# Optimization experiments

Measured on AMD Instinct MI355X. Metric: run time of the kernel, lower is better.

The kernel has to match this reference:

```python
import jax, jax.numpy as jnp
import numpy as np
import math

WINDOW_SIZE = 1024
CAUSAL = True


def setup_inputs() -> dict:
    key = jax.random.key(0)
    kq, kk, kv = jax.random.split(key, 3)
    B, H, L, D = 2, 16, 4096, 128
    q = jax.random.normal(kq, (B, H, L, D), dtype=jnp.float32)
    k = jax.random.normal(kk, (B, H, L, D), dtype=jnp.float32)
    v = jax.random.normal(kv, (B, H, L, D), dtype=jnp.float32)
    return {"q": q, "k": k, "v": v}


def _sliding_window_attention(q, k, v):
    # Faithful port of SlidingWindowAttention._blockwise_attention (L > 2048 path).
    B, H, L, D = q.shape
    block = min(WINDOW_SIZE, 1024)
    scale = 1.0 / math.sqrt(D)
    half_w = WINDOW_SIZE // 2
    outs = []
    # Python loop over a small fixed number of blocks (L/block = 4), not data dims.
    for s in range(0, L, block):
        e = min(s + block, L)
        ks = max(0, s - half_w)
        ke = min(L, e + half_w)
        if CAUSAL:
            ke = min(ke, e)
        qb = q[:, :, s:e, :]          # [B,H,Q,D]
        kb = k[:, :, ks:ke, :]        # [B,H,K,D]
        vb = v[:, :, ks:ke, :]        # [B,H,K,D]
        scores = jnp.einsum('bhqd,bhkd->bhqk', qb, kb) * scale
        if CAUSAL:
            qi = jnp.arange(s, e)[:, None]   # [Q,1]
            ki = jnp.arange(ks, ke)[None, :]  # [1,K]
            causal_mask = qi >= ki            # [Q,K]
            scores = jnp.where(causal_mask[None, None], scores, -jnp.inf)
        attn = jax.nn.softmax(scores, axis=-1)
        outs.append(jnp.einsum('bhqk,bhkd->bhqd', attn, vb))
    return jnp.concatenate(outs, axis=2)


def reference(q, k, v):
    return _sliding_window_attention(q, k, v)
```

## Files before the change

kernel.cpp:

```cpp
#include <hip/hip_runtime.h>
#include <hip/hip_bf16.h>
#include <stdint.h>

typedef __bf16 bf16_t;
typedef __bf16 bf16x8 __attribute__((ext_vector_type(8)));
typedef __bf16 bf16x4 __attribute__((ext_vector_type(4)));
typedef float f32x4 __attribute__((ext_vector_type(4)));

#define L_SEQ 4096
#define D_DIM 128
#define NBH   32
#define KT    64

__global__ __launch_bounds__(256)
void cvt_k(const float* __restrict__ Kg, bf16_t* __restrict__ Kws) {
    const int n   = blockIdx.x * 256 + threadIdx.x;
    const int key = n >> 4;
    const int pc  = n & 15;
    const int lc  = pc ^ (key & 7);
    const float* s = Kg + (size_t)key * D_DIM + lc * 8;
    f32x4 a = *(const f32x4*)(s);
    f32x4 b = *(const f32x4*)(s + 4);
    bf16x8 h;
    #pragma unroll
    for (int j = 0; j < 4; ++j) { h[j] = (bf16_t)a[j]; h[4 + j] = (bf16_t)b[j]; }
    *(bf16x8*)(Kws + (size_t)key * D_DIM + pc * 8) = h;
}

__global__ __launch_bounds__(256)
void cvt_v(const float* __restrict__ Vg, bf16_t* __restrict__ Vws) {
    const int blk  = blockIdx.x;
    const int bh   = blk >> 6;
    const int kb   = blk & 63;
    const int t    = threadIdx.x;
    const int d    = t & 127;
    const int half = t >> 7;
    const float* src0 = Vg + (size_t)(bh * L_SEQ + kb * 64) * D_DIM + d;
    bf16_t* dstrow = Vws + ((size_t)(bh * 64 + kb) * D_DIM + d) * 64;
    #pragma unroll
    for (int r2 = 0; r2 < 4; ++r2) {
        const int lc = half + 2 * r2;
        bf16x8 h;
        #pragma unroll
        for (int j = 0; j < 8; ++j)
            h[j] = (bf16_t)src0[(size_t)(lc * 8 + j) * D_DIM];
        const int pc = lc ^ (d & 7);
        *(bf16x8*)(&dstrow[pc * 8]) = h;
    }
}

__device__ __forceinline__ void ld_lds16(const void* g, void* s) {
    __builtin_amdgcn_global_load_lds(
        (const __attribute__((address_space(1))) unsigned int*)g,
        (__attribute__((address_space(3))) unsigned int*)s, 16, 0, 0);
}

#define QT2 128

__global__ __launch_bounds__(256, 2)
void swa_fwd2(const float* __restrict__ Qg,
              const bf16_t* __restrict__ Kws,
              const bf16_t* __restrict__ Vws,
              float* __restrict__ Og) {
    __shared__ __align__(16) bf16_t KtS[2][KT * D_DIM];
    __shared__ __align__(16) bf16_t VtS[2][D_DIM * KT];
    __shared__ __align__(16) bf16_t Pst[4][16 * KT];

    const int t    = threadIdx.x;
    const int w    = t >> 6;
    const int ln   = t & 15;
    const int quad = (t & 63) >> 4;
    const int l7   = t & 7;

    const int id = blockIdx.x;
    const int bh = id & 31;
    const int g  = id >> 5;
    const int r_ = g & 7;
    const int k_ = g >> 3;
    const int qt = 8 * k_ + ((k_ & 1) ? (7 - r_) : r_);

    const size_t baseF = (size_t)bh * L_SEQ * D_DIM;
    const float*  Qp = Qg + baseF;
    float*        Op = Og + baseF;
    const bf16_t* Kb = Kws + baseF;
    const bf16_t* Vb = Vws + (size_t)bh * 64 * D_DIM * 64;

    const int qbase  = qt * QT2;
    const int blk    = qbase & ~1023;
    const int kstart = (blk - 512) > 0 ? (blk - 512) : 0;
    const int kend   = qbase + QT2;
    const int ntile  = (kend - kstart) / KT;

    const float SC  = 0.08838834764831845f * 1.4426950408889634f;
    const float FIX = 8.0f;
    const float NEG = -1.0e30f;

    bf16x8 qf[2][4];
    #pragma unroll
    for (int mt = 0; mt < 2; ++mt) {
        const float* qrow = Qp + (size_t)(qbase + w * 32 + mt * 16 + ln) * D_DIM + quad * 8;
        #pragma unroll
        for (int ks = 0; ks < 4; ++ks) {
            f32x4 a = *(const f32x4*)(qrow + ks * 32);
            f32x4 b = *(const f32x4*)(qrow + ks * 32 + 4);
            bf16x8 q8;
            #pragma unroll
            for (int j = 0; j < 4; ++j) { q8[j] = (bf16_t)(a[j] * SC); q8[4 + j] = (bf16_t)(b[j] * SC); }
            qf[mt][ks] = q8;
        }
    }

    f32x4 Oacc[2][8];
    #pragma unroll
    for (int mt = 0; mt < 2; ++mt)
        #pragma unroll
        for (int dt = 0; dt < 8; ++dt) Oacc[mt][dt] = f32x4{0.f, 0.f, 0.f, 0.f};
    float lsum[2] = {0.f, 0.f};

    auto stage = [&](int b, int k0) {
        const char* ksrc = (const char*)Kb + (size_t)k0 * 256;
        const char* vsrc = (const char*)Vb + (size_t)(k0 >> 6) * 16384;
        char* kd = (char*)(&KtS[b][0]);
        char* vd = (char*)(&VtS[b][0]);
        #pragma unroll
        for (int i = 0; i < 4; ++i) {
            const int off = (i * 256 + t) * 16;
            ld_lds16(ksrc + off, kd + off);
            ld_lds16(vsrc + off, vd + off);
        }
    };

    stage(0, kstart);
    __syncthreads();

    int buf = 0;
    for (int kt = 0; kt < ntile; ++kt) {
        const int k0 = kstart + kt * KT;
        if (kt + 1 < ntile) stage(buf ^ 1, k0 + KT);

        f32x4 S[2][4];
        #pragma unroll
        for (int mt = 0; mt < 2; ++mt)
            #pragma unroll
            for (int nt = 0; nt < 4; ++nt) S[mt][nt] = f32x4{0.f, 0.f, 0.f, 0.f};
        #pragma unroll
        for (int ks = 0; ks < 4; ++ks) {
            #pragma unroll
            for (int nt = 0; nt < 4; ++nt) {
                const bf16x8 bk = *(const bf16x8*)(
                    &KtS[buf][(nt * 16 + ln) * D_DIM + (((quad + ks * 4) ^ l7) * 8)]);
                S[0][nt] = __builtin_amdgcn_mfma_f32_16x16x32_bf16(bk, qf[0][ks], S[0][nt], 0, 0, 0);
                S[1][nt] = __builtin_amdgcn_mfma_f32_16x16x32_bf16(bk, qf[1][ks], S[1][nt], 0, 0, 0);
            }
        }

        bf16x8 pa[2][2];
        #pragma unroll
        for (int mt = 0; mt < 2; ++mt) {
            const int qwm = qbase + w * 32 + mt * 16;
            const int qg  = qwm + ln;
            const bool nm = (k0 + KT - 1) > qwm;
            #pragma unroll
            for (int nt = 0; nt < 4; ++nt) {
                bf16x4 hp;
                #pragma unroll
                for (int r = 0; r < 4; ++r) {
                    float s = S[mt][nt][r];
                    if (nm) {
                        const int kg = k0 + nt * 16 + quad * 4 + r;
                        if (kg > qg) s = NEG;
                    }
                    const float e = __builtin_amdgcn_exp2f(s - FIX);
                    lsum[mt] += e;
                    hp[r] = (bf16_t)e;
                }
                *(bf16x4*)(&Pst[w][ln * 64 + (((nt * 2 + (quad >> 1)) ^ l7) * 8) + (quad & 1) * 4]) = hp;
            }
            #pragma unroll
            for (int ks2 = 0; ks2 < 2; ++ks2)
                pa[mt][ks2] = *(const bf16x8*)(
                    &Pst[w][ln * 64 + (((quad + ks2 * 4) ^ l7) * 8)]);
        }

        #pragma unroll
        for (int dt = 0; dt < 8; ++dt) {
            #pragma unroll
            for (int ks2 = 0; ks2 < 2; ++ks2) {
                const bf16x8 bv = *(const bf16x8*)(
                    &VtS[buf][(dt * 16 + ln) * 64 + (((quad + ks2 * 4) ^ l7) * 8)]);
                Oacc[0][dt] = __builtin_amdgcn_mfma_f32_16x16x32_bf16(bv, pa[0][ks2], Oacc[0][dt], 0, 0, 0);
                Oacc[1][dt] = __builtin_amdgcn_mfma_f32_16x16x32_bf16(bv, pa[1][ks2], Oacc[1][dt], 0, 0, 0);
            }
        }

        __syncthreads();
        buf ^= 1;
    }

    #pragma unroll
    for (int mt = 0; mt < 2; ++mt) {
        float l = lsum[mt];
        l += __shfl_xor(l, 16, 64);
        l += __shfl_xor(l, 32, 64);
        const float inv = (l > 0.f) ? (1.f / l) : 0.f;
        const int qg = qbase + w * 32 + mt * 16 + ln;
        float* orow = Op + (size_t)qg * D_DIM + quad * 4;
        #pragma unroll
        for (int dt = 0; dt < 8; ++dt) {
            f32x4 o = Oacc[mt][dt];
            #pragma unroll
            for (int j = 0; j < 4; ++j) o[j] *= inv;
            *(f32x4*)(orow + dt * 16) = o;
        }
    }
}

#define QT 64
#define LDK 136
#define LDV 72
#define LDP 72

__global__ __launch_bounds__(256, 2)
void swa_fwd(const float* __restrict__ Qg,
             const float* __restrict__ Kg,
             const float* __restrict__ Vg,
             float* __restrict__ Og) {
    __shared__ __align__(16) bf16_t Kt[KT][LDK];
    __shared__ __align__(16) bf16_t Vt[D_DIM][LDV];
    __shared__ __align__(16) bf16_t Pstf[4][16][LDP];

    const int t    = threadIdx.x;
    const int w    = t >> 6;
    const int ln   = t & 15;
    const int quad = (t & 63) >> 4;

    const int id = blockIdx.x;
    const int bh = id & 31;
    const int g  = id >> 5;
    const int q0 = g & 7;
    const int kk = g >> 3;
    const int qt = 16 * (kk >> 1) + ((kk & 1) ? (15 - q0) : q0);

    const size_t base = (size_t)bh * L_SEQ * D_DIM;
    const float* Qp = Qg + base;
    const float* Kp = Kg + base;
    const float* Vp = Vg + base;
    float*       Op = Og + base;

    const int qbase  = qt * QT;
    const int blk    = qbase & ~1023;
    const int kstart = (blk - 512) > 0 ? (blk - 512) : 0;
    const int kend   = qbase + QT;
    const int ntile  = (kend - kstart) / KT;

    const int qw = qbase + w * 16;

    const float SC  = 0.08838834764831845f * 1.4426950408889634f;
    const float FIX = 8.0f;

    bf16x8 qf[4];
    {
        const float* qrow = Qp + (size_t)(qw + ln) * D_DIM + quad * 8;
        #pragma unroll
        for (int ks = 0; ks < 4; ++ks) {
            f32x4 a = *(const f32x4*)(qrow + ks * 32);
            f32x4 b = *(const f32x4*)(qrow + ks * 32 + 4);
            bf16x8 q8;
            #pragma unroll
            for (int j = 0; j < 4; ++j) {
                q8[j]     = (bf16_t)(a[j] * SC);
                q8[4 + j] = (bf16_t)(b[j] * SC);
            }
            qf[ks] = q8;
        }
    }

    f32x4 Oacc[8];
    #pragma unroll
    for (int dt = 0; dt < 8; ++dt) Oacc[dt] = f32x4{0.f, 0.f, 0.f, 0.f};
    float lsum[4] = {0.f, 0.f, 0.f, 0.f};
    const float NEG = -1.0e30f;

    const int kr   = t >> 5;
    const int kc   = t & 31;
    const int vd   = t & 127;
    const int vkcb = t >> 7;

    f32x4 kreg[8];
    float vreg[4][8];

    auto load_tile = [&](int k0) {
        #pragma unroll
        for (int i = 0; i < 8; ++i)
            kreg[i] = *(const f32x4*)(Kp + (size_t)(k0 + kr + 8 * i) * D_DIM + kc * 4);
        #pragma unroll
        for (int r2 = 0; r2 < 4; ++r2) {
            const int kcc = vkcb + 2 * r2;
            #pragma unroll
            for (int j = 0; j < 8; ++j)
                vreg[r2][j] = Vp[(size_t)(k0 + kcc * 8 + j) * D_DIM + vd];
        }
    };
    auto store_tile = [&]() {
        #pragma unroll
        for (int i = 0; i < 8; ++i) {
            bf16x4 h;
            #pragma unroll
            for (int j = 0; j < 4; ++j) h[j] = (bf16_t)kreg[i][j];
            *(bf16x4*)(&Kt[kr + 8 * i][kc * 4]) = h;
        }
        #pragma unroll
        for (int r2 = 0; r2 < 4; ++r2) {
            const int kcc = vkcb + 2 * r2;
            bf16x8 h8;
            #pragma unroll
            for (int j = 0; j < 8; ++j) h8[j] = (bf16_t)vreg[r2][j];
            *(bf16x8*)(&Vt[vd][kcc * 8]) = h8;
        }
    };

    load_tile(kstart);

    for (int kt = 0; kt < ntile; ++kt) {
        const int k0 = kstart + kt * KT;
        __syncthreads();
        store_tile();
        __syncthreads();
        if (kt + 1 < ntile) load_tile(k0 + KT);

        f32x4 S[4];
        #pragma unroll
        for (int nt = 0; nt < 4; ++nt) S[nt] = f32x4{0.f, 0.f, 0.f, 0.f};
        #pragma unroll
        for (int ks = 0; ks < 4; ++ks) {
            #pragma unroll
            for (int nt = 0; nt < 4; ++nt) {
                bf16x8 bk = *(const bf16x8*)(&Kt[nt * 16 + ln][quad * 8 + ks * 32]);
                S[nt] = __builtin_amdgcn_mfma_f32_16x16x32_bf16(qf[ks], bk, S[nt], 0, 0, 0);
            }
        }

        const bool lastTile = (kt == ntile - 1);
        float p[4][4];
        #pragma unroll
        for (int nt = 0; nt < 4; ++nt) {
            #pragma unroll
            for (int r = 0; r < 4; ++r) {
                float s = S[nt][r];
                if (lastTile) {
                    const int kg = k0 + nt * 16 + ln;
                    const int qg = qw + quad * 4 + r;
                    if (kg > qg) s = NEG;
                }
                const float e = __builtin_amdgcn_exp2f(s - FIX);
                p[nt][r] = e;
                lsum[r] += e;
            }
        }

        #pragma unroll
        for (int nt = 0; nt < 4; ++nt)
            #pragma unroll
            for (int r = 0; r < 4; ++r)
                Pstf[w][quad * 4 + r][nt * 16 + ln] = (bf16_t)p[nt][r];

        bf16x8 pa[2];
        #pragma unroll
        for (int ks2 = 0; ks2 < 2; ++ks2)
            pa[ks2] = *(const bf16x8*)(&Pstf[w][ln][quad * 8 + ks2 * 32]);

        #pragma unroll
        for (int dt = 0; dt < 8; ++dt) {
            #pragma unroll
            for (int ks2 = 0; ks2 < 2; ++ks2) {
                bf16x8 bv = *(const bf16x8*)(&Vt[dt * 16 + ln][quad * 8 + ks2 * 32]);
                Oacc[dt] = __builtin_amdgcn_mfma_f32_16x16x32_bf16(pa[ks2], bv, Oacc[dt], 0, 0, 0);
            }
        }
    }

    #pragma unroll
    for (int r = 0; r < 4; ++r) {
        float l = lsum[r];
        #pragma unroll
        for (int msk = 1; msk < 16; msk <<= 1)
            l += __shfl_xor(l, msk, 64);
        const float inv = (l > 0.f) ? (1.f / l) : 0.f;
        const int qg = qw + quad * 4 + r;
        float* orow = Op + (size_t)qg * D_DIM + ln;
        #pragma unroll
        for (int dt = 0; dt < 8; ++dt)
            orow[dt * 16] = Oacc[dt][r] * inv;
    }
}

extern "C" void kernel_launch(void* const* d_in, const int* in_sizes, int n_in,
                              void* d_out, int out_size, void* d_ws, size_t ws_size,
                              hipStream_t stream) {
    const float* q = (const float*)d_in[0];
    const float* k = (const float*)d_in[1];
    const float* v = (const float*)d_in[2];
    float* o = (float*)d_out;

    const size_t kbytes = (size_t)NBH * L_SEQ * D_DIM * sizeof(bf16_t);
    if (d_ws && ws_size >= 2 * kbytes) {
        bf16_t* kws = (bf16_t*)d_ws;
        bf16_t* vws = (bf16_t*)((char*)d_ws + kbytes);
        cvt_k<<<dim3(8192), dim3(256), 0, stream>>>(k, kws);
        cvt_v<<<dim3(2048), dim3(256), 0, stream>>>(v, vws);
        swa_fwd2<<<dim3(1024), dim3(256), 0, stream>>>(q, kws, vws, o);
    } else {
        swa_fwd<<<dim3(2048), dim3(256), 0, stream>>>(q, k, v, o);
    }
}
```

Baseline: 306.8 us.

## Shrink key tile to 32, raise occupancy, skip fully masked wave tiles

Halves the key tile from 64 to 32 keys. This shrinks the shared-memory footprint and register pressure so four blocks per CU can be requested instead of two, and the V pre-transpose layout and its swizzle are changed to match. Each wave now skips compute on key tiles lying entirely above its causal diagonal, and MFMA phases are wrapped in s_setprio to favour matrix issue. The cost is twice as many tile iterations and barriers per block, with smaller staging loads that hide less latency per sync.

```diff
diff --git a/kernel.cpp b/kernel.cpp
--- a/kernel.cpp
+++ b/kernel.cpp
@@ -10,7 +10,7 @@
 #define L_SEQ 4096
 #define D_DIM 128
 #define NBH   32
-#define KT    64
+#define KT    32
 
 __global__ __launch_bounds__(256)
 void cvt_k(const float* __restrict__ Kg, bf16_t* __restrict__ Kws) {
@@ -30,22 +30,22 @@
 __global__ __launch_bounds__(256)
 void cvt_v(const float* __restrict__ Vg, bf16_t* __restrict__ Vws) {
     const int blk  = blockIdx.x;
-    const int bh   = blk >> 6;
-    const int kb   = blk & 63;
+    const int bh   = blk >> 7;
+    const int kb   = blk & 127;
     const int t    = threadIdx.x;
     const int d    = t & 127;
     const int half = t >> 7;
-    const float* src0 = Vg + (size_t)(bh * L_SEQ + kb * 64) * D_DIM + d;
-    bf16_t* dstrow = Vws + ((size_t)(bh * 64 + kb) * D_DIM + d) * 64;
-    #pragma unroll
-    for (int r2 = 0; r2 < 4; ++r2) {
+    const float* src0 = Vg + (size_t)(bh * L_SEQ + kb * 32) * D_DIM + d;
+    bf16_t* dstrow = Vws + ((size_t)(bh * 128 + kb) * D_DIM + d) * 32;
+    const int sw = (d >> 1) & 3;
+    #pragma unroll
+    for (int r2 = 0; r2 < 2; ++r2) {
         const int lc = half + 2 * r2;
         bf16x8 h;
         #pragma unroll
         for (int j = 0; j < 8; ++j)
             h[j] = (bf16_t)src0[(size_t)(lc * 8 + j) * D_DIM];
-        const int pc = lc ^ (d & 7);
-        *(bf16x8*)(&dstrow[pc * 8]) = h;
+        *(bf16x8*)(&dstrow[(lc ^ sw) * 8]) = h;
     }
 }
 
@@ -57,8 +57,8 @@
 
 #define QT2 128
 
-__global__ __launch_bounds__(256, 2)
-void swa_fwd2(const float* __restrict__ Qg,
+__global__ __launch_bounds__(256, 4)
+void swa_fwd3(const float* __restrict__ Qg,
               const bf16_t* __restrict__ Kws,
               const bf16_t* __restrict__ Vws,
               float* __restrict__ Og) {
@@ -83,7 +83,7 @@
     const float*  Qp = Qg + baseF;
     float*        Op = Og + baseF;
     const bf16_t* Kb = Kws + baseF;
-    const bf16_t* Vb = Vws + (size_t)bh * 64 * D_DIM * 64;
+    const bf16_t* Vb = Vws + (size_t)bh * 128 * D_DIM * 32;
 
     const int qbase  = qt * QT2;
     const int blk    = qbase & ~1023;
@@ -91,6 +91,9 @@
     const int kend   = qbase + QT2;
     const int ntile  = (kend - kstart) / KT;
 
+    const int qw    = qbase + w * 32;
+    const int qwmax = qw + 31;
+
     const float SC  = 0.08838834764831845f * 1.4426950408889634f;
     const float FIX = 8.0f;
     const float NEG = -1.0e30f;
@@ -98,7 +101,7 @@
     bf16x8 qf[2][4];
     #pragma unroll
     for (int mt = 0; mt < 2; ++mt) {
-        const float* qrow = Qp + (size_t)(qbase + w * 32 + mt * 16 + ln) * D_DIM + quad * 8;
+        const float* qrow = Qp + (size_t)(qw + mt * 16 + ln) * D_DIM + quad * 8;
         #pragma unroll
         for (int ks = 0; ks < 4; ++ks) {
             f32x4 a = *(const f32x4*)(qrow + ks * 32);
@@ -119,11 +122,11 @@
 
     auto stage = [&](int b, int k0) {
         const char* ksrc = (const char*)Kb + (size_t)k0 * 256;
-        const char* vsrc = (const char*)Vb + (size_t)(k0 >> 6) * 16384;
+        const char* vsrc = (const char*)Vb + (size_t)(k0 >> 5) * 8192;
         char* kd = (char*)(&KtS[b][0]);
         char* vd = (char*)(&VtS[b][0]);
         #pragma unroll
-        for (int i = 0; i < 4; ++i) {
+        for (int i = 0; i < 2; ++i) {
             const int off = (i * 256 + t) * 16;
             ld_lds16(ksrc + off, kd + off);
             ld_lds16(vsrc + off, vd + off);
@@ -138,59 +141,60 @@
         const int k0 = kstart + kt * KT;
         if (kt + 1 < ntile) stage(buf ^ 1, k0 + KT);
 
-        f32x4 S[2][4];
-        #pragma unroll
-        for (int mt = 0; mt < 2; ++mt)
-            #pragma unroll
-            for (int nt = 0; nt < 4; ++nt) S[mt][nt] = f32x4{0.f, 0.f, 0.f, 0.f};
-        #pragma unroll
-        for (int ks = 0; ks < 4; ++ks) {
-            #pragma unroll
-            for (int nt = 0; nt < 4; ++nt) {
-                const bf16x8 bk = *(const bf16x8*)(
-                    &KtS[buf][(nt * 16 + ln) * D_DIM + (((quad + ks * 4) ^ l7) * 8)]);
-                S[0][nt] = __builtin_amdgcn_mfma_f32_16x16x32_bf16(bk, qf[0][ks], S[0][nt], 0, 0, 0);
-                S[1][nt] = __builtin_amdgcn_mfma_f32_16x16x32_bf16(bk, qf[1][ks], S[1][nt], 0, 0, 0);
-            }
-        }
-
-        bf16x8 pa[2][2];
-        #pragma unroll
-        for (int mt = 0; mt < 2; ++mt) {
-            const int qwm = qbase + w * 32 + mt * 16;
-            const int qg  = qwm + ln;
-            const bool nm = (k0 + KT - 1) > qwm;
-            #pragma unroll
-            for (int nt = 0; nt < 4; ++nt) {
-                bf16x4 hp;
+        if (k0 <= qwmax) {
+            f32x4 S[2][2];
+            #pragma unroll
+            for (int mt = 0; mt < 2; ++mt)
                 #pragma unroll
-                for (int r = 0; r < 4; ++r) {
-                    float s = S[mt][nt][r];
-                    if (nm) {
-                        const int kg = k0 + nt * 16 + quad * 4 + r;
-                        if (kg > qg) s = NEG;
+                for (int nt = 0; nt < 2; ++nt) S[mt][nt] = f32x4{0.f, 0.f, 0.f, 0.f};
+            __builtin_amdgcn_s_setprio(1);
+            #pragma unroll
+            for (int ks = 0; ks < 4; ++ks) {
+                #pragma unroll
+                for (int nt = 0; nt < 2; ++nt) {
+                    const bf16x8 bk = *(const bf16x8*)(
+                        &KtS[buf][(nt * 16 + ln) * D_DIM + (((ks * 4 + quad) ^ l7) * 8)]);
+                    S[0][nt] = __builtin_amdgcn_mfma_f32_16x16x32_bf16(bk, qf[0][ks], S[0][nt], 0, 0, 0);
+                    S[1][nt] = __builtin_amdgcn_mfma_f32_16x16x32_bf16(bk, qf[1][ks], S[1][nt], 0, 0, 0);
+                }
+            }
+            __builtin_amdgcn_s_setprio(0);
+
+            bf16x8 pa[2];
+            #pragma unroll
+            for (int mt = 0; mt < 2; ++mt) {
+                const int qwm = qw + mt * 16;
+                const int qg  = qwm + ln;
+                const bool nm = (k0 + KT - 1) > qwm;
+                #pragma unroll
+                for (int nt = 0; nt < 2; ++nt) {
+                    bf16x4 hp;
+                    #pragma unroll
+                    for (int r = 0; r < 4; ++r) {
+                        float s = S[mt][nt][r];
+                        if (nm) {
+                            const int kg = k0 + nt * 16 + quad * 4 + r;
+                            if (kg > qg) s = NEG;
+                        }
+                        const float e = __builtin_amdgcn_exp2f(s - FIX);
+                        lsum[mt] += e;
+                        hp[r] = (bf16_t)e;
                     }
-                    const float e = __builtin_amdgcn_exp2f(s - FIX);
-                    lsum[mt] += e;
-                    hp[r] = (bf16_t)e;
+                    *(bf16x4*)(&Pst[w][ln * KT +
+                        (((nt * 2 + (quad >> 1)) ^ (ln & 3)) * 8) + (quad & 1) * 4]) = hp;
                 }
-                *(bf16x4*)(&Pst[w][ln * 64 + (((nt * 2 + (quad >> 1)) ^ l7) * 8) + (quad & 1) * 4]) = hp;
-            }
-            #pragma unroll
-            for (int ks2 = 0; ks2 < 2; ++ks2)
-                pa[mt][ks2] = *(const bf16x8*)(
-                    &Pst[w][ln * 64 + (((quad + ks2 * 4) ^ l7) * 8)]);
-        }
-
-        #pragma unroll
-        for (int dt = 0; dt < 8; ++dt) {
-            #pragma unroll
-            for (int ks2 = 0; ks2 < 2; ++ks2) {
+                pa[mt] = *(const bf16x8*)(&Pst[w][ln * KT + ((quad ^ (ln & 3)) * 8)]);
+            }
+
+            __builtin_amdgcn_s_setprio(1);
+            #pragma unroll
+            for (int dt = 0; dt < 8; ++dt) {
                 const bf16x8 bv = *(const bf16x8*)(
-                    &VtS[buf][(dt * 16 + ln) * 64 + (((quad + ks2 * 4) ^ l7) * 8)]);
-                Oacc[0][dt] = __builtin_amdgcn_mfma_f32_16x16x32_bf16(bv, pa[0][ks2], Oacc[0][dt], 0, 0, 0);
-                Oacc[1][dt] = __builtin_amdgcn_mfma_f32_16x16x32_bf16(bv, pa[1][ks2], Oacc[1][dt], 0, 0, 0);
-            }
+                    &VtS[buf][(dt * 16 + ln) * KT + ((quad ^ ((ln >> 1) & 3)) * 8)]);
+                Oacc[0][dt] = __builtin_amdgcn_mfma_f32_16x16x32_bf16(bv, pa[0], Oacc[0][dt], 0, 0, 0);
+                Oacc[1][dt] = __builtin_amdgcn_mfma_f32_16x16x32_bf16(bv, pa[1], Oacc[1][dt], 0, 0, 0);
+            }
+            __builtin_amdgcn_s_setprio(0);
         }
 
         __syncthreads();
@@ -203,7 +207,7 @@
         l += __shfl_xor(l, 16, 64);
         l += __shfl_xor(l, 32, 64);
         const float inv = (l > 0.f) ? (1.f / l) : 0.f;
-        const int qg = qbase + w * 32 + mt * 16 + ln;
+        const int qg = qw + mt * 16 + ln;
         float* orow = Op + (size_t)qg * D_DIM + quad * 4;
         #pragma unroll
         for (int dt = 0; dt < 8; ++dt) {
@@ -215,7 +219,8 @@
     }
 }
 
-#define QT 64
+#define QTF 64
+#define KTF 64
 #define LDK 136
 #define LDV 72
 #define LDP 72
@@ -225,7 +230,7 @@
              const float* __restrict__ Kg,
              const float* __restrict__ Vg,
              float* __restrict__ Og) {
-    __shared__ __align__(16) bf16_t Kt[KT][LDK];
+    __shared__ __align__(16) bf16_t Kt[KTF][LDK];
     __shared__ __align__(16) bf16_t Vt[D_DIM][LDV];
     __shared__ __align__(16) bf16_t Pstf[4][16][LDP];
 
@@ -247,11 +252,11 @@
     const float* Vp = Vg + base;
     float*       Op = Og + base;
 
-    const int qbase  = qt * QT;
+    const int qbase  = qt * QTF;
     const int blk    = qbase & ~1023;
     const int kstart = (blk - 512) > 0 ? (blk - 512) : 0;
-    const int kend   = qbase + QT;
-    const int ntile  = (kend - kstart) / KT;
+    const int kend   = qbase + QTF;
+    const int ntile  = (kend - kstart) / KTF;
 
     const int qw = qbase + w * 16;
 
@@ -322,11 +327,11 @@
     load_tile(kstart);
 
     for (int kt = 0; kt < ntile; ++kt) {
-        const int k0 = kstart + kt * KT;
+        const int k0 = kstart + kt * KTF;
         __syncthreads();
         store_tile();
         __syncthreads();
-        if (kt + 1 < ntile) load_tile(k0 + KT);
+        if (kt + 1 < ntile) load_tile(k0 + KTF);
 
         f32x4 S[4];
         #pragma unroll
@@ -407,8 +412,8 @@
         bf16_t* kws = (bf16_t*)d_ws;
         bf16_t* vws = (bf16_t*)((char*)d_ws + kbytes);
         cvt_k<<<dim3(8192), dim3(256), 0, stream>>>(k, kws);
-        cvt_v<<<dim3(2048), dim3(256), 0, stream>>>(v, vws);
-        swa_fwd2<<<dim3(1024), dim3(256), 0, stream>>>(q, kws, vws, o);
+        cvt_v<<<dim3(4096), dim3(256), 0, stream>>>(v, vws);
+        swa_fwd3<<<dim3(1024), dim3(256), 0, stream>>>(q, kws, vws, o);
     } else {
         swa_fwd<<<dim3(2048), dim3(256), 0, stream>>>(q, k, v, o);
     }
```

Result: slower. 358.7 us (+16.9%).
